# Performance work log

Measured on AMD Instinct MI355X. Metric: run time of the kernel, lower is better.

Reference implementation:

```python
import jax, jax.numpy as jnp
import numpy as np

BIG = 1e6  # diagonal mask value from the original module


def setup_inputs() -> dict:
    key = jax.random.key(0)
    k1, k2, k3 = jax.random.split(key, 3)
    B, D = 16384, 128
    return {
        "query_embeddings": jax.random.normal(k1, (B, D), dtype=jnp.float32),
        "doc_embeddings": jax.random.normal(k2, (B, D), dtype=jnp.float32),
        "neg_doc_embeddings": jax.random.normal(k3, (B, D), dtype=jnp.float32),
    }


def reference(query_embeddings, doc_embeddings, neg_doc_embeddings):
    # Pairwise term: diagonal of q @ d.T is just a row-wise dot product.
    pos_scores = jnp.einsum("bd,bd->b", query_embeddings, doc_embeddings)
    neg_scores = jnp.einsum("bd,bd->b", query_embeddings, neg_doc_embeddings)
    loss = jax.nn.softplus(neg_scores - pos_scores).mean()

    # In-batch hardest-negative term (in_batch_term=True): full [B, B] scores.
    scores = jnp.einsum("bd,cd->bc", query_embeddings, doc_embeddings)
    B = scores.shape[0]
    idx = jnp.arange(B)
    pos_ib = scores[idx, idx]
    # subtract 1e6 on the diagonal (same as original: scores - eye * 1e6)
    neg_ib = scores.at[idx, idx].add(-BIG).max(axis=1)
    loss = loss + jax.nn.softplus(neg_ib - pos_ib).mean()

    return loss / 2
```

## Files before the change

kernel.cpp:

```cpp
#include <hip/hip_runtime.h>
#include <hip/hip_bf16.h>


#define BATCH 16384
#define DDIM  128
#define NWAVES 4
#define ROWS_PER_BLOCK 256
#define COLS_PER_BLOCK 1024
#define CHUNK_COLS 64
#define NCHUNKS (COLS_PER_BLOCK / CHUNK_COLS)
#define CHUNK_USHORTS (CHUNK_COLS * DDIM)
#define NCG (BATCH / COLS_PER_BLOCK)
#define NRG (BATCH / ROWS_PER_BLOCK)
#define NPREP 2048
#define NRED  64

typedef __attribute__((ext_vector_type(8))) short bf16x8;
typedef __attribute__((ext_vector_type(4))) float f32x4;

__device__ __forceinline__ float softplus_f(float x) {
    return (x > 0.0f) ? x + log1pf(expf(-x)) : log1pf(expf(x));
}

__device__ __forceinline__ ushort f2bf_rne(float x) {
    unsigned u = __float_as_uint(x);
    unsigned r = (u + 0x7FFFu + ((u >> 16) & 1u)) >> 16;
    return (ushort)r;
}

#define WAITVM(n) do { \
        __builtin_amdgcn_s_waitcnt((n) | (7 << 4) | (15 << 8)); \
        asm volatile("" ::: "memory"); \
    } while (0)

__global__ __launch_bounds__(256) void prep_kernel(
    const float* __restrict__ q, const float* __restrict__ d,
    const float* __restrict__ nd,
    ushort* __restrict__ qb, ushort* __restrict__ db,
    float* __restrict__ pos, float* __restrict__ loss1_part)
{
    const int t   = threadIdx.x;
    const int sub = t >> 5;
    const int ln  = t & 31;
    const int row = blockIdx.x * 8 + sub;
    const size_t idx = (size_t)row * DDIM + ln * 4;

    float4 a = *(const float4*)(q  + idx);
    float4 b = *(const float4*)(d  + idx);
    float4 c = *(const float4*)(nd + idx);

    ushort4 o;
    o.x = f2bf_rne(a.x); o.y = f2bf_rne(a.y);
    o.z = f2bf_rne(a.z); o.w = f2bf_rne(a.w);
    *(ushort4*)(qb + idx) = o;
    ushort4 p;
    p.x = f2bf_rne(b.x); p.y = f2bf_rne(b.y);
    p.z = f2bf_rne(b.z); p.w = f2bf_rne(b.w);
    *(ushort4*)(db + idx) = p;

    float ps = a.x * b.x + a.y * b.y + a.z * b.z + a.w * b.w;
    float ns = a.x * c.x + a.y * c.y + a.z * c.z + a.w * c.w;
    ps += __shfl_xor(ps, 1); ps += __shfl_xor(ps, 2);
    ps += __shfl_xor(ps, 4); ps += __shfl_xor(ps, 8);
    ps += __shfl_xor(ps, 16);
    ns += __shfl_xor(ns, 1); ns += __shfl_xor(ns, 2);
    ns += __shfl_xor(ns, 4); ns += __shfl_xor(ns, 8);
    ns += __shfl_xor(ns, 16);

    float contrib = 0.0f;
    if (ln == 0) {
        pos[row] = ps;
        contrib = softplus_f(ns - ps);
    }
    contrib += __shfl_xor(contrib, 32);

    __shared__ float red[4];
    if ((t & 63) == 0) red[t >> 6] = contrib;
    __syncthreads();
    if (t == 0)
        loss1_part[blockIdx.x] = red[0] + red[1] + red[2] + red[3];
}

__global__ __launch_bounds__(256, 2) void inbatch_kernel(
    const ushort* __restrict__ qb, const ushort* __restrict__ db,
    float* __restrict__ partials)
{
    __shared__ ushort stg[2][CHUNK_USHORTS];

    const int t      = threadIdx.x;
    const int w      = t >> 6;
    const int l      = t & 63;
    const int lane16 = l & 15;
    const int quad   = l >> 4;
    const int rg     = blockIdx.x & 63;
    const int cg     = blockIdx.x >> 6;
    const int rows0  = rg * ROWS_PER_BLOCK + w * 64;
    const int col0   = cg * COLS_PER_BLOCK;

    bf16x8 afrag[4][4];
#pragma unroll
    for (int rs = 0; rs < 4; ++rs)
#pragma unroll
        for (int ks = 0; ks < 4; ++ks)
            afrag[rs][ks] = *(const bf16x8*)(
                qb + (size_t)(rows0 + rs * 16 + lane16) * DDIM + ks * 32 + quad * 8);

    const ushort* gsrc[4];
#pragma unroll
    for (int i = 0; i < 4; ++i) {
        int c = i * 16 + (t >> 4);
        gsrc[i] = db + (size_t)(col0 + c) * DDIM + (((t & 15) ^ ((t >> 4) & 15)) * 8);
    }

    int dsbase[4];
#pragma unroll
    for (int ks = 0; ks < 4; ++ks)
        dsbase[ks] = lane16 * DDIM + (((ks * 4 + quad) ^ lane16) * 8);

    float runmax[4][4];
#pragma unroll
    for (int rs = 0; rs < 4; ++rs)
#pragma unroll
        for (int r = 0; r < 4; ++r) runmax[rs][r] = -3.0e38f;

#pragma unroll
    for (int i = 0; i < 4; ++i)
        __builtin_amdgcn_global_load_lds(
            (const __attribute__((address_space(1))) void*)gsrc[i],
            (__attribute__((address_space(3))) void*)(&stg[0][0] + (i * 256 + w * 64) * 8),
            16, 0, 0);

    for (int ch = 0; ch < NCHUNKS; ++ch) {
        WAITVM(0);
        __syncthreads();
        if (ch + 1 < NCHUNKS) {
#pragma unroll
            for (int i = 0; i < 4; ++i)
                __builtin_amdgcn_global_load_lds(
                    (const __attribute__((address_space(1))) void*)(gsrc[i] + (size_t)(ch + 1) * CHUNK_USHORTS),
                    (__attribute__((address_space(3))) void*)(&stg[(ch + 1) & 1][0] + (i * 256 + w * 64) * 8),
                    16, 0, 0);
        }

        const ushort* buf = &stg[ch & 1][0];
#pragma unroll
        for (int ct = 0; ct < 4; ++ct) {
            bf16x8 bfrag[4];
#pragma unroll
            for (int ks = 0; ks < 4; ++ks)
                bfrag[ks] = *(const bf16x8*)(buf + dsbase[ks] + ct * 2048);

            const int ctile = col0 + ch * CHUNK_COLS + ct * 16;
#pragma unroll
            for (int rs = 0; rs < 4; ++rs) {
                f32x4 s = {0.0f, 0.0f, 0.0f, 0.0f};
#pragma unroll
                for (int ks = 0; ks < 4; ++ks)
                    s = __builtin_amdgcn_mfma_f32_16x16x32_bf16(
                        afrag[rs][ks], bfrag[ks], s, 0, 0, 0);
                if (ctile == rows0 + rs * 16) {
#pragma unroll
                    for (int r = 0; r < 4; ++r)
                        if (quad * 4 + r == lane16) s[r] -= 1.0e6f;
                }
#pragma unroll
                for (int r = 0; r < 4; ++r)
                    runmax[rs][r] = fmaxf(runmax[rs][r], s[r]);
            }
        }
    }

#pragma unroll
    for (int rs = 0; rs < 4; ++rs)
#pragma unroll
        for (int r = 0; r < 4; ++r) {
            float m = runmax[rs][r];
            m = fmaxf(m, __shfl_xor(m, 1));
            m = fmaxf(m, __shfl_xor(m, 2));
            m = fmaxf(m, __shfl_xor(m, 4));
            m = fmaxf(m, __shfl_xor(m, 8));
            runmax[rs][r] = m;
        }

    if (lane16 == 0) {
#pragma unroll
        for (int rs = 0; rs < 4; ++rs)
#pragma unroll
            for (int r = 0; r < 4; ++r)
                partials[(size_t)cg * BATCH + rows0 + rs * 16 + quad * 4 + r] =
                    runmax[rs][r];
    }
}

__global__ __launch_bounds__(256) void reduce_kernel(
    const float* __restrict__ partials, const float* __restrict__ pos,
    float* __restrict__ red_part)
{
    const int t = threadIdx.x;
    const int r = blockIdx.x * 256 + t;
    float fm = partials[r];
#pragma unroll
    for (int cgi = 1; cgi < NCG; ++cgi)
        fm = fmaxf(fm, partials[(size_t)cgi * BATCH + r]);
    float c = softplus_f(fm - pos[r]);
    c += __shfl_xor(c, 1);  c += __shfl_xor(c, 2);
    c += __shfl_xor(c, 4);  c += __shfl_xor(c, 8);
    c += __shfl_xor(c, 16); c += __shfl_xor(c, 32);

    __shared__ float red[4];
    if ((t & 63) == 0) red[t >> 6] = c;
    __syncthreads();
    if (t == 0)
        red_part[blockIdx.x] = red[0] + red[1] + red[2] + red[3];
}

__global__ __launch_bounds__(256) void finalize_kernel(
    const float* __restrict__ loss1_part, const float* __restrict__ red_part,
    float* __restrict__ out)
{
    const int t = threadIdx.x;
    float s = 0.0f;
#pragma unroll
    for (int i = 0; i < NPREP / 256; ++i)
        s += loss1_part[i * 256 + t];
    if (t < NRED) s += red_part[t];
    s += __shfl_xor(s, 1);  s += __shfl_xor(s, 2);
    s += __shfl_xor(s, 4);  s += __shfl_xor(s, 8);
    s += __shfl_xor(s, 16); s += __shfl_xor(s, 32);

    __shared__ float red[4];
    if ((t & 63) == 0) red[t >> 6] = s;
    __syncthreads();
    if (t == 0)
        out[0] = (red[0] + red[1] + red[2] + red[3]) * (1.0f / (2.0f * BATCH));
}

extern "C" void kernel_launch(void* const* d_in, const int* in_sizes, int n_in,
                              void* d_out, int out_size, void* d_ws, size_t ws_size,
                              hipStream_t stream)
{
    const float* q  = (const float*)d_in[0];
    const float* d  = (const float*)d_in[1];
    const float* nd = (const float*)d_in[2];
    float* out = (float*)d_out;

    char* ws = (char*)d_ws;
    float*  pos        = (float*)ws;
    ushort* qb         = (ushort*)(ws + 65536);
    ushort* db         = (ushort*)(ws + 65536 + 4194304);
    float*  partials   = (float*)(ws + 65536 + 2 * 4194304);
    float*  loss1_part = (float*)(ws + 65536 + 2 * 4194304 + 1048576);
    float*  red_part   = (float*)(ws + 65536 + 2 * 4194304 + 1048576 + 8192);

    prep_kernel<<<NPREP, 256, 0, stream>>>(q, d, nd, qb, db, pos, loss1_part);
    inbatch_kernel<<<NRG * NCG, 256, 0, stream>>>(qb, db, partials);
    reduce_kernel<<<NRED, 256, 0, stream>>>(partials, pos, red_part);
    finalize_kernel<<<1, 256, 0, stream>>>(loss1_part, red_part, out);
}
```

Baseline: 129.5 us.

## Load B fragments directly from global into registers, dropping LDS staging

Removes the shared-memory double-buffered staging of doc tiles (global_load_lds plus barriers). Each wave now reads its B fragments straight from global/L2 into registers, with a two-tile software register prefetch. This is meant to eliminate the per-chunk barriers and LDS read traffic. In exchange, each of the four waves in a block reloads the same doc tile from cache, multiplying global/L2 traffic, and the launch-bounds occupancy hint is dropped.

```diff
diff --git a/kernel.cpp b/kernel.cpp
--- a/kernel.cpp
+++ b/kernel.cpp
@@ -4,12 +4,9 @@
 
 #define BATCH 16384
 #define DDIM  128
-#define NWAVES 4
 #define ROWS_PER_BLOCK 256
 #define COLS_PER_BLOCK 1024
-#define CHUNK_COLS 64
-#define NCHUNKS (COLS_PER_BLOCK / CHUNK_COLS)
-#define CHUNK_USHORTS (CHUNK_COLS * DDIM)
+#define NTILES (COLS_PER_BLOCK / 16)
 #define NCG (BATCH / COLS_PER_BLOCK)
 #define NRG (BATCH / ROWS_PER_BLOCK)
 #define NPREP 2048
@@ -27,11 +24,6 @@
     unsigned r = (u + 0x7FFFu + ((u >> 16) & 1u)) >> 16;
     return (ushort)r;
 }
-
-#define WAITVM(n) do { \
-        __builtin_amdgcn_s_waitcnt((n) | (7 << 4) | (15 << 8)); \
-        asm volatile("" ::: "memory"); \
-    } while (0)
 
 __global__ __launch_bounds__(256) void prep_kernel(
     const float* __restrict__ q, const float* __restrict__ d,
@@ -81,12 +73,10 @@
         loss1_part[blockIdx.x] = red[0] + red[1] + red[2] + red[3];
 }
 
-__global__ __launch_bounds__(256, 2) void inbatch_kernel(
+__global__ __launch_bounds__(256) void inbatch_kernel(
     const ushort* __restrict__ qb, const ushort* __restrict__ db,
     float* __restrict__ partials)
 {
-    __shared__ ushort stg[2][CHUNK_USHORTS];
-
     const int t      = threadIdx.x;
     const int w      = t >> 6;
     const int l      = t & 63;
@@ -105,70 +95,57 @@
             afrag[rs][ks] = *(const bf16x8*)(
                 qb + (size_t)(rows0 + rs * 16 + lane16) * DDIM + ks * 32 + quad * 8);
 
-    const ushort* gsrc[4];
-#pragma unroll
-    for (int i = 0; i < 4; ++i) {
-        int c = i * 16 + (t >> 4);
-        gsrc[i] = db + (size_t)(col0 + c) * DDIM + (((t & 15) ^ ((t >> 4) & 15)) * 8);
+    const ushort* bp = db + (size_t)(col0 + lane16) * DDIM + quad * 8;
+
+    float runmax[4][4];
+#pragma unroll
+    for (int rs = 0; rs < 4; ++rs)
+#pragma unroll
+        for (int r = 0; r < 4; ++r) runmax[rs][r] = -3.0e38f;
+
+    const f32x4 zinit = {0.0f, 0.0f, 0.0f, 0.0f};
+
+#define LOAD_B(dst, j)                                                     \
+    do {                                                                   \
+        _Pragma("unroll")                                                  \
+        for (int ks = 0; ks < 4; ++ks)                                     \
+            dst[ks] = *(const bf16x8*)(bp + (size_t)(j) * 2048 + ks * 32); \
+    } while (0)
+
+#define PROC_B(src, j)                                                     \
+    do {                                                                   \
+        const int ctile = col0 + (j) * 16;                                 \
+        _Pragma("unroll")                                                  \
+        for (int rs = 0; rs < 4; ++rs) {                                   \
+            f32x4 s = __builtin_amdgcn_mfma_f32_16x16x32_bf16(             \
+                afrag[rs][0], src[0], zinit, 0, 0, 0);                     \
+            _Pragma("unroll")                                              \
+            for (int ks = 1; ks < 4; ++ks)                                 \
+                s = __builtin_amdgcn_mfma_f32_16x16x32_bf16(               \
+                    afrag[rs][ks], src[ks], s, 0, 0, 0);                   \
+            if (ctile == rows0 + rs * 16) {       \
+                _Pragma("unroll")                                          \
+                for (int r = 0; r < 4; ++r)                                \
+                    if (quad * 4 + r == lane16) s[r] -= 1.0e6f;            \
+            }                                                              \
+            _Pragma("unroll")                                              \
+            for (int r = 0; r < 4; ++r)                                    \
+                runmax[rs][r] = fmaxf(runmax[rs][r], s[r]);                \
+        }                                                                  \
+    } while (0)
+
+    bf16x8 bf0[4], bf1[4];
+    LOAD_B(bf0, 0);
+    LOAD_B(bf1, 1);
+
+    for (int u = 0; u < NTILES / 2; ++u) {
+        PROC_B(bf0, 2 * u);
+        if (u + 1 < NTILES / 2) LOAD_B(bf0, 2 * u + 2);
+        PROC_B(bf1, 2 * u + 1);
+        if (u + 1 < NTILES / 2) LOAD_B(bf1, 2 * u + 3);
     }
-
-    int dsbase[4];
-#pragma unroll
-    for (int ks = 0; ks < 4; ++ks)
-        dsbase[ks] = lane16 * DDIM + (((ks * 4 + quad) ^ lane16) * 8);
-
-    float runmax[4][4];
-#pragma unroll
-    for (int rs = 0; rs < 4; ++rs)
-#pragma unroll
-        for (int r = 0; r < 4; ++r) runmax[rs][r] = -3.0e38f;
-
-#pragma unroll
-    for (int i = 0; i < 4; ++i)
-        __builtin_amdgcn_global_load_lds(
-            (const __attribute__((address_space(1))) void*)gsrc[i],
-            (__attribute__((address_space(3))) void*)(&stg[0][0] + (i * 256 + w * 64) * 8),
-            16, 0, 0);
-
-    for (int ch = 0; ch < NCHUNKS; ++ch) {
-        WAITVM(0);
-        __syncthreads();
-        if (ch + 1 < NCHUNKS) {
-#pragma unroll
-            for (int i = 0; i < 4; ++i)
-                __builtin_amdgcn_global_load_lds(
-                    (const __attribute__((address_space(1))) void*)(gsrc[i] + (size_t)(ch + 1) * CHUNK_USHORTS),
-                    (__attribute__((address_space(3))) void*)(&stg[(ch + 1) & 1][0] + (i * 256 + w * 64) * 8),
-                    16, 0, 0);
-        }
-
-        const ushort* buf = &stg[ch & 1][0];
-#pragma unroll
-        for (int ct = 0; ct < 4; ++ct) {
-            bf16x8 bfrag[4];
-#pragma unroll
-            for (int ks = 0; ks < 4; ++ks)
-                bfrag[ks] = *(const bf16x8*)(buf + dsbase[ks] + ct * 2048);
-
-            const int ctile = col0 + ch * CHUNK_COLS + ct * 16;
-#pragma unroll
-            for (int rs = 0; rs < 4; ++rs) {
-                f32x4 s = {0.0f, 0.0f, 0.0f, 0.0f};
-#pragma unroll
-                for (int ks = 0; ks < 4; ++ks)
-                    s = __builtin_amdgcn_mfma_f32_16x16x32_bf16(
-                        afrag[rs][ks], bfrag[ks], s, 0, 0, 0);
-                if (ctile == rows0 + rs * 16) {
-#pragma unroll
-                    for (int r = 0; r < 4; ++r)
-                        if (quad * 4 + r == lane16) s[r] -= 1.0e6f;
-                }
-#pragma unroll
-                for (int r = 0; r < 4; ++r)
-                    runmax[rs][r] = fmaxf(runmax[rs][r], s[r]);
-            }
-        }
-    }
+#undef LOAD_B
+#undef PROC_B
 
 #pragma unroll
     for (int rs = 0; rs < 4; ++rs)
```

Result: slower. 199.9 us (+54.4%).

## Switch in-batch GEMM to 32x32x16 MFMA and fold final reduction into atomics

Applied to the files above, without the earlier changes.

Replaces the 16x16x32 bf16 MFMA tiling in the in-batch kernel with 32x32x16 MFMA tiles. This changes the A/B fragment layouts, the LDS swizzle, the diagonal masking and the row-max reduction to match the 32-wide output layout. The larger tile is meant to cut LDS fragment reads per FLOP and use the denser MFMA shape, at the cost of more accumulator registers; the launch_bounds min-blocks hint is dropped. The finalize kernel is removed: prep and reduce now atomically add scaled partial sums into the output after a memset. This saves one launch but makes the float summation order nondeterministic.

```diff
diff --git a/kernel.cpp b/kernel.cpp
--- a/kernel.cpp
+++ b/kernel.cpp
@@ -4,7 +4,6 @@
 
 #define BATCH 16384
 #define DDIM  128
-#define NWAVES 4
 #define ROWS_PER_BLOCK 256
 #define COLS_PER_BLOCK 1024
 #define CHUNK_COLS 64
@@ -14,9 +13,10 @@
 #define NRG (BATCH / ROWS_PER_BLOCK)
 #define NPREP 2048
 #define NRED  64
+#define SCALE (1.0f / (2.0f * BATCH))
 
 typedef __attribute__((ext_vector_type(8))) short bf16x8;
-typedef __attribute__((ext_vector_type(4))) float f32x4;
+typedef __attribute__((ext_vector_type(16))) float f32x16;
 
 __device__ __forceinline__ float softplus_f(float x) {
     return (x > 0.0f) ? x + log1pf(expf(-x)) : log1pf(expf(x));
@@ -37,7 +37,7 @@
     const float* __restrict__ q, const float* __restrict__ d,
     const float* __restrict__ nd,
     ushort* __restrict__ qb, ushort* __restrict__ db,
-    float* __restrict__ pos, float* __restrict__ loss1_part)
+    float* __restrict__ pos, float* __restrict__ out)
 {
     const int t   = threadIdx.x;
     const int sub = t >> 5;
@@ -78,50 +78,55 @@
     if ((t & 63) == 0) red[t >> 6] = contrib;
     __syncthreads();
     if (t == 0)
-        loss1_part[blockIdx.x] = red[0] + red[1] + red[2] + red[3];
-}
-
-__global__ __launch_bounds__(256, 2) void inbatch_kernel(
+        atomicAdd(out, (red[0] + red[1] + red[2] + red[3]) * SCALE);
+}
+
+__global__ __launch_bounds__(256) void inbatch_kernel(
     const ushort* __restrict__ qb, const ushort* __restrict__ db,
     float* __restrict__ partials)
 {
     __shared__ ushort stg[2][CHUNK_USHORTS];
 
-    const int t      = threadIdx.x;
-    const int w      = t >> 6;
-    const int l      = t & 63;
-    const int lane16 = l & 15;
-    const int quad   = l >> 4;
-    const int rg     = blockIdx.x & 63;
-    const int cg     = blockIdx.x >> 6;
-    const int rows0  = rg * ROWS_PER_BLOCK + w * 64;
-    const int col0   = cg * COLS_PER_BLOCK;
-
-    bf16x8 afrag[4][4];
-#pragma unroll
-    for (int rs = 0; rs < 4; ++rs)
-#pragma unroll
-        for (int ks = 0; ks < 4; ++ks)
-            afrag[rs][ks] = *(const bf16x8*)(
-                qb + (size_t)(rows0 + rs * 16 + lane16) * DDIM + ks * 32 + quad * 8);
+    const int t     = threadIdx.x;
+    const int w     = t >> 6;
+    const int l     = t & 63;
+    const int col32 = l & 31;
+    const int half  = l >> 5;
+    const int rg    = blockIdx.x & 63;
+    const int cg    = blockIdx.x >> 6;
+    const int rows0 = rg * ROWS_PER_BLOCK + w * 64;
+    const int col0  = cg * COLS_PER_BLOCK;
+
+    bf16x8 afrag[2][8];
+#pragma unroll
+    for (int rs = 0; rs < 2; ++rs)
+#pragma unroll
+        for (int kk = 0; kk < 8; ++kk)
+            afrag[rs][kk] = *(const bf16x8*)(
+                qb + (size_t)(rows0 + rs * 32 + col32) * DDIM + kk * 16 + half * 8);
 
     const ushort* gsrc[4];
 #pragma unroll
     for (int i = 0; i < 4; ++i) {
-        int c = i * 16 + (t >> 4);
-        gsrc[i] = db + (size_t)(col0 + c) * DDIM + (((t & 15) ^ ((t >> 4) & 15)) * 8);
-    }
-
-    int dsbase[4];
-#pragma unroll
-    for (int ks = 0; ks < 4; ++ks)
-        dsbase[ks] = lane16 * DDIM + (((ks * 4 + quad) ^ lane16) * 8);
-
-    float runmax[4][4];
-#pragma unroll
-    for (int rs = 0; rs < 4; ++rs)
-#pragma unroll
-        for (int r = 0; r < 4; ++r) runmax[rs][r] = -3.0e38f;
+        int seg = i * 256 + t;
+        int c   = seg >> 4;
+        int s   = seg & 15;
+        gsrc[i] = db + (size_t)(col0 + c) * DDIM + ((s ^ (c & 15)) * 8);
+    }
+
+    int dsbase[8];
+#pragma unroll
+    for (int kk = 0; kk < 8; ++kk)
+        dsbase[kk] = col32 * DDIM + (((kk * 2 + half) ^ (col32 & 15)) * 8);
+
+    float runmax[2][16];
+#pragma unroll
+    for (int rs = 0; rs < 2; ++rs)
+#pragma unroll
+        for (int r = 0; r < 16; ++r) runmax[rs][r] = -3.0e38f;
+
+    const f32x16 zinit = {0.0f,0.0f,0.0f,0.0f,0.0f,0.0f,0.0f,0.0f,
+                          0.0f,0.0f,0.0f,0.0f,0.0f,0.0f,0.0f,0.0f};
 
 #pragma unroll
     for (int i = 0; i < 4; ++i)
@@ -144,57 +149,61 @@
 
         const ushort* buf = &stg[ch & 1][0];
 #pragma unroll
-        for (int ct = 0; ct < 4; ++ct) {
-            bf16x8 bfrag[4];
-#pragma unroll
-            for (int ks = 0; ks < 4; ++ks)
-                bfrag[ks] = *(const bf16x8*)(buf + dsbase[ks] + ct * 2048);
-
-            const int ctile = col0 + ch * CHUNK_COLS + ct * 16;
-#pragma unroll
-            for (int rs = 0; rs < 4; ++rs) {
-                f32x4 s = {0.0f, 0.0f, 0.0f, 0.0f};
-#pragma unroll
-                for (int ks = 0; ks < 4; ++ks)
-                    s = __builtin_amdgcn_mfma_f32_16x16x32_bf16(
-                        afrag[rs][ks], bfrag[ks], s, 0, 0, 0);
-                if (ctile == rows0 + rs * 16) {
-#pragma unroll
-                    for (int r = 0; r < 4; ++r)
-                        if (quad * 4 + r == lane16) s[r] -= 1.0e6f;
+        for (int ct = 0; ct < 2; ++ct) {
+            bf16x8 bfrag[8];
+#pragma unroll
+            for (int kk = 0; kk < 8; ++kk)
+                bfrag[kk] = *(const bf16x8*)(buf + dsbase[kk] + ct * 4096);
+
+            const int ctile = col0 + ch * CHUNK_COLS + ct * 32;
+#pragma unroll
+            for (int rs = 0; rs < 2; ++rs) {
+                f32x16 s = __builtin_amdgcn_mfma_f32_32x32x16_bf16(
+                    afrag[rs][0], bfrag[0], zinit, 0, 0, 0);
+#pragma unroll
+                for (int kk = 1; kk < 8; ++kk)
+                    s = __builtin_amdgcn_mfma_f32_32x32x16_bf16(
+                        afrag[rs][kk], bfrag[kk], s, 0, 0, 0);
+                if (ctile == rows0 + rs * 32) {
+#pragma unroll
+                    for (int r = 0; r < 16; ++r) {
+                        int row = (r & 3) + 8 * (r >> 2) + 4 * half;
+                        if (row == col32) s[r] -= 1.0e6f;
+                    }
                 }
 #pragma unroll
-                for (int r = 0; r < 4; ++r)
+                for (int r = 0; r < 16; ++r)
                     runmax[rs][r] = fmaxf(runmax[rs][r], s[r]);
             }
         }
     }
 
 #pragma unroll
-    for (int rs = 0; rs < 4; ++rs)
-#pragma unroll
-        for (int r = 0; r < 4; ++r) {
+    for (int rs = 0; rs < 2; ++rs)
+#pragma unroll
+        for (int r = 0; r < 16; ++r) {
             float m = runmax[rs][r];
             m = fmaxf(m, __shfl_xor(m, 1));
             m = fmaxf(m, __shfl_xor(m, 2));
             m = fmaxf(m, __shfl_xor(m, 4));
             m = fmaxf(m, __shfl_xor(m, 8));
+            m = fmaxf(m, __shfl_xor(m, 16));
             runmax[rs][r] = m;
         }
 
-    if (lane16 == 0) {
-#pragma unroll
-        for (int rs = 0; rs < 4; ++rs)
-#pragma unroll
-            for (int r = 0; r < 4; ++r)
-                partials[(size_t)cg * BATCH + rows0 + rs * 16 + quad * 4 + r] =
-                    runmax[rs][r];
+    if (col32 == 0) {
+#pragma unroll
+        for (int rs = 0; rs < 2; ++rs)
+#pragma unroll
+            for (int r = 0; r < 16; ++r)
+                partials[(size_t)cg * BATCH + rows0 + rs * 32
+                         + (r & 3) + 8 * (r >> 2) + 4 * half] = runmax[rs][r];
     }
 }
 
 __global__ __launch_bounds__(256) void reduce_kernel(
     const float* __restrict__ partials, const float* __restrict__ pos,
-    float* __restrict__ red_part)
+    float* __restrict__ out)
 {
     const int t = threadIdx.x;
     const int r = blockIdx.x * 256 + t;
@@ -211,28 +220,7 @@
     if ((t & 63) == 0) red[t >> 6] = c;
     __syncthreads();
     if (t == 0)
-        red_part[blockIdx.x] = red[0] + red[1] + red[2] + red[3];
-}
-
-__global__ __launch_bounds__(256) void finalize_kernel(
-    const float* __restrict__ loss1_part, const float* __restrict__ red_part,
-    float* __restrict__ out)
-{
-    const int t = threadIdx.x;
-    float s = 0.0f;
-#pragma unroll
-    for (int i = 0; i < NPREP / 256; ++i)
-        s += loss1_part[i * 256 + t];
-    if (t < NRED) s += red_part[t];
-    s += __shfl_xor(s, 1);  s += __shfl_xor(s, 2);
-    s += __shfl_xor(s, 4);  s += __shfl_xor(s, 8);
-    s += __shfl_xor(s, 16); s += __shfl_xor(s, 32);
-
-    __shared__ float red[4];
-    if ((t & 63) == 0) red[t >> 6] = s;
-    __syncthreads();
-    if (t == 0)
-        out[0] = (red[0] + red[1] + red[2] + red[3]) * (1.0f / (2.0f * BATCH));
+        atomicAdd(out, (red[0] + red[1] + red[2] + red[3]) * SCALE);
 }
 
 extern "C" void kernel_launch(void* const* d_in, const int* in_sizes, int n_in,
@@ -245,15 +233,13 @@
     float* out = (float*)d_out;
 
     char* ws = (char*)d_ws;
-    float*  pos        = (float*)ws;
-    ushort* qb         = (ushort*)(ws + 65536);
-    ushort* db         = (ushort*)(ws + 65536 + 4194304);
-    float*  partials   = (float*)(ws + 65536 + 2 * 4194304);
-    float*  loss1_part = (float*)(ws + 65536 + 2 * 4194304 + 1048576);
-    float*  red_part   = (float*)(ws + 65536 + 2 * 4194304 + 1048576 + 8192);
-
-    prep_kernel<<<NPREP, 256, 0, stream>>>(q, d, nd, qb, db, pos, loss1_part);
+    float*  pos      = (float*)ws;
+    ushort* qb       = (ushort*)(ws + 65536);
+    ushort* db       = (ushort*)(ws + 65536 + 4194304);
+    float*  partials = (float*)(ws + 65536 + 2 * 4194304);
+
+    hipMemsetAsync(out, 0, sizeof(float), stream);
+    prep_kernel<<<NPREP, 256, 0, stream>>>(q, d, nd, qb, db, pos, out);
     inbatch_kernel<<<NRG * NCG, 256, 0, stream>>>(qb, db, partials);
-    reduce_kernel<<<NRED, 256, 0, stream>>>(partials, pos, red_part);
-    finalize_kernel<<<1, 256, 0, stream>>>(loss1_part, red_part, out);
-}
+    reduce_kernel<<<NRED, 256, 0, stream>>>(partials, pos, out);
+}
```

After: 163.8 us. 1.27x slower.
